# Optimization experiments

Measured on AMD Instinct MI355X. Metric: run time of the kernel, lower is better.

## Reference

```python
import jax, jax.numpy as jnp
import numpy as np

# --- static forest structure: NT complete ternary trees of depth DEPTH ---
BR, DEPTH, NT = 3, 7, 64            # branching factor (=L), edge-levels, num trees
OFF = [(3 ** d - 1) // 2 for d in range(DEPTH + 2)]  # BFS level offsets within a tree
NPT = OFF[DEPTH + 1]                 # nodes per tree = 3280
DIM = NT * NPT                       # total nodes = 209920
C_DIM, NGEN, M_SYM = 8, 8, 128


def build_tree():
    """Returns pos, leaves, batch, roots, levels [(parent_idx, child_idx)], unique-parents per level."""
    base = (np.arange(NT) * NPT)[:, None]
    pos = np.zeros(DIM, dtype=np.int64)
    levels, upar = [], []
    for d in range(1, DEPTH + 1):
        loc = np.arange(OFF[d], OFF[d + 1])
        ch = (base + loc).ravel()                                 # children at depth d (tree-major)
        pa = (base + (OFF[d - 1] + (loc - OFF[d]) // BR)).ravel() # their parents
        pos[ch] = np.tile((loc - OFF[d]) % BR, NT)
        levels.append((pa, ch))
        upar.append((base + np.arange(OFF[d - 1], OFF[d])).ravel())  # unique parents of level d
    leaves = (base + np.arange(OFF[DEPTH], OFF[DEPTH + 1])).ravel()
    batch = np.repeat(np.arange(NT), NPT)
    roots = np.arange(NT) * NPT
    return pos, leaves, batch, roots, levels, upar


def setup_inputs() -> dict:
    key = jax.random.key(0)
    k1, k2, k3, k4, k5 = jax.random.split(key, 5)
    pos_np, leaves_np, batch_np, _, _, _ = build_tree()
    return {
        "lam_A": jax.random.uniform(k1, (C_DIM, C_DIM, BR, NGEN), dtype=jnp.float32),
        "lam_B": jax.random.uniform(k2, (C_DIM, M_SYM, NGEN), dtype=jnp.float32),
        "lam_Pi": jax.random.uniform(k3, (C_DIM, BR, NGEN), dtype=jnp.float32),
        "lam_SP": jax.random.uniform(k4, (BR, NGEN), dtype=jnp.float32),
        "x": jax.random.randint(k5, (DIM,), 0, M_SYM, dtype=jnp.int64),
        "pos": jnp.asarray(pos_np),
        "leaves": jnp.asarray(leaves_np),
        "batch": jnp.asarray(batch_np),
    }


def reference(lam_A, lam_B, lam_Pi, lam_SP, x, pos, leaves, batch):
    # ReversedUpwardDownward (mode='bu') of PosteriorHiddenTreeMarkovModel.
    A = jax.nn.softmax(lam_A, axis=0)   # (C,C,L,G): softmax over first state axis
    Bm = jax.nn.softmax(lam_B, axis=1)  # (C,M,G): softmax over symbols
    Pi = jax.nn.softmax(lam_Pi, axis=0) # (C,L,G)
    SP = jax.nn.softmax(lam_SP, axis=0) # (L,G)
    C, G = A.shape[0], A.shape[-1]
    _, _, _, roots, levels, upar = build_tree()  # static structure

    beta = jnp.zeros((DIM, C, G), lam_A.dtype)
    t_beta = jnp.zeros((DIM, C, G), lam_A.dtype)

    # --- leaves init ---
    Pi_leaves = Pi[:, pos[leaves]]            # (C,Nl,G)
    bl = jnp.transpose(Pi_leaves * Bm[:, x[leaves]], (1, 0, 2))  # (Nl,C,G)
    beta = beta.at[leaves].set(bl / bl.sum(1, keepdims=True))

    # --- upward pass (deepest level first) ---
    for (pa, ch), u in zip(reversed(levels), reversed(upar)):
        SP_ch = SP[pos[ch]][:, None, None, :]                 # (E,1,1,G)
        A_ch = jnp.transpose(A[:, :, pos[ch]], (2, 0, 1, 3))  # (E,C,C,G)
        tb = (SP_ch * A_ch * beta[ch][:, None]).sum(2)        # (E,C,G) sum over child state
        t_beta = t_beta.at[pa].add(tb)
        bu = t_beta[u] * jnp.transpose(Bm[:, x[u]], (1, 0, 2))
        beta = beta.at[u].set(bu / bu.sum(1, keepdims=True))

    # --- downward pass ---
    eps = jnp.zeros((DIM, C, G), lam_A.dtype)
    ell = jnp.zeros((DIM, G), lam_A.dtype)
    eps = eps.at[roots].set(beta[roots])
    for pa, ch in levels:
        SP_ch = SP[pos[ch]]                                   # (E,G)
        A_ch = jnp.transpose(A[:, :, pos[ch]], (2, 0, 1, 3))  # (E,C,C,G)
        trans = SP_ch[:, None, None, :] * A_ch
        ej = (eps[pa][:, :, None, :] * trans * beta[ch][:, None, :, :]
              / t_beta[pa][:, :, None, :])                    # (E,C,C,G) joint posterior
        eps = eps.at[ch].set(ej.sum(1))
        ell = ell.at[ch].add((ej * jnp.log(A_ch)).sum((1, 2))
                             + ej.sum((1, 2)) * jnp.log(SP_ch))
    ell = ell + (eps * jnp.transpose(Bm[:, x], (1, 0, 2))).sum(1)
    ell = ell.at[leaves].add((eps[leaves] * jnp.transpose(jnp.log(Pi_leaves), (1, 0, 2))).sum(1))
    return -jax.ops.segment_sum(ell, batch, num_segments=NT)  # (NT,G)
```

## Files before the change

### kernel.cpp

```cpp
#include <hip/hip_runtime.h>


namespace {

constexpr int kNPT = 3280;
constexpr int kRS  = 72;
constexpr unsigned kMAGIC  = 0x13579BDFu;
constexpr unsigned kMAGIC2 = 0x2468ACEFu;
__device__ __constant__ int LO[6] = {0, 1, 4, 13, 40, 121};
__device__ __constant__ int P3[5] = {1, 3, 9, 27, 81};

#define AGENT_LD(p)    __hip_atomic_load((p), __ATOMIC_RELAXED, __HIP_MEMORY_SCOPE_AGENT)
#define AGENT_ST(p, v) __hip_atomic_store((p), (v), __ATOMIC_RELAXED, __HIP_MEMORY_SCOPE_AGENT)

__device__ __forceinline__ void leaf_beta(const float* __restrict__ sPi,
                                          const float* __restrict__ pBm,
                                          int p, int xv, int g, float* b)
{
    float s = 0.f;
    #pragma unroll
    for (int c = 0; c < 8; ++c) {
        b[c] = sPi[(c * 3 + p) * 8 + g] * pBm[xv * 64 + c * 8 + g];
        s += b[c];
    }
    float ig = __builtin_amdgcn_rcpf(s);
    #pragma unroll
    for (int c = 0; c < 8; ++c) b[c] *= ig;
}

__global__ __launch_bounds__(256, 2)
void fused(const float* __restrict__ lamA, const float* __restrict__ lamB,
           const float* __restrict__ lamPi, const float* __restrict__ lamSP,
           const int* __restrict__ x, float* __restrict__ out,
           unsigned* __restrict__ sy, float* __restrict__ bmG,
           float* __restrict__ b3, float* __restrict__ e3)
{
    const int tid = threadIdx.x, w = tid >> 6, lane = tid & 63;
    const int n = lane >> 3, g = lane & 7;
    __shared__ float sA[1536], sALA[1536], sPi[192], sLPi[192], sSP[24], sLSP[24];
    __shared__ float bW[4][40 * kRS];
    __shared__ float bMid[13 * kRS];
    __shared__ unsigned char xW[4][124];
    unsigned* trCnt = sy + 32;
    unsigned* trFlg = sy + 2080;

    if (tid == 0) {
        if (blockIdx.x == 0) {
            for (int i = 0; i < 64; ++i) AGENT_ST(&trCnt[i * 32], 0u);
            __builtin_amdgcn_s_waitcnt(0);
            AGENT_ST(&sy[0], kMAGIC);
        }
        unsigned long sp = 0;
        while (AGENT_LD(&sy[0]) != kMAGIC) {
            if (++sp > (1UL << 24)) break;
            __builtin_amdgcn_s_sleep(2);
        }
    }
    __syncthreads();

    if (blockIdx.x == 0) {
        float* rr = &bW[0][0];
        int row = tid >> 2, part = tid & 3;
        int c = row >> 3, gg = row & 7, m0 = part * 32;
        float mx = -1e30f;
        for (int mm = 0; mm < 32; ++mm)
            mx = fmaxf(mx, lamB[(c * 128 + m0 + mm) * 8 + gg]);
        rr[tid] = mx;
        __syncthreads();
        float m4 = fmaxf(fmaxf(rr[row * 4], rr[row * 4 + 1]),
                         fmaxf(rr[row * 4 + 2], rr[row * 4 + 3]));
        float s = 0.f;
        for (int mm = 0; mm < 32; ++mm)
            s += expf(lamB[(c * 128 + m0 + mm) * 8 + gg] - m4);
        rr[256 + tid] = s;
        __syncthreads();
        float stot = rr[256 + row * 4] + rr[256 + row * 4 + 1]
                   + rr[256 + row * 4 + 2] + rr[256 + row * 4 + 3];
        float inv = 1.f / stot;
        for (int mm = 0; mm < 32; ++mm)
            AGENT_ST(&bmG[(m0 + mm) * 64 + c * 8 + gg],
                     expf(lamB[(c * 128 + m0 + mm) * 8 + gg] - m4) * inv);
        __syncthreads();
        if (tid == 0) AGENT_ST(&sy[4], kMAGIC2);
    }
    for (int col = tid; col < 192; col += 256) {
        int j = col / 24; int rem = col - j * 24; int p = rem >> 3; int gg = rem & 7;
        float v[8]; float mx = -1e30f;
        #pragma unroll
        for (int i = 0; i < 8; ++i) {
            v[i] = lamA[((i * 8 + j) * 3 + p) * 8 + gg];
            mx = fmaxf(mx, v[i]);
        }
        float s = 0.f;
        #pragma unroll
        for (int i = 0; i < 8; ++i) { v[i] = expf(v[i] - mx); s += v[i]; }
        float inv = 1.f / s;
        #pragma unroll
        for (int i = 0; i < 8; ++i) {
            int idx = ((i * 8 + j) * 3 + p) * 8 + gg;
            float sm = v[i] * inv;
            sA[idx]   = sm;
            sALA[idx] = sm * logf(sm);
        }
    }
    for (int col = tid; col < 24; col += 256) {
        int p = col >> 3; int gg = col & 7;
        float v[8]; float mx = -1e30f;
        #pragma unroll
        for (int c = 0; c < 8; ++c) {
            v[c] = lamPi[(c * 3 + p) * 8 + gg];
            mx = fmaxf(mx, v[c]);
        }
        float s = 0.f;
        #pragma unroll
        for (int c = 0; c < 8; ++c) { v[c] = expf(v[c] - mx); s += v[c]; }
        float inv = 1.f / s;
        #pragma unroll
        for (int c = 0; c < 8; ++c) {
            int idx = (c * 3 + p) * 8 + gg;
            float sm = v[c] * inv;
            sPi[idx]  = sm;
            sLPi[idx] = logf(sm);
        }
    }
    if (tid < 8) {
        int gg = tid;
        float v0 = lamSP[gg], v1 = lamSP[8 + gg], v2 = lamSP[16 + gg];
        float mx = fmaxf(v0, fmaxf(v1, v2));
        float e0 = expf(v0 - mx), e1 = expf(v1 - mx), e2 = expf(v2 - mx);
        float inv = 1.f / (e0 + e1 + e2);
        sSP[gg] = e0 * inv; sSP[8 + gg] = e1 * inv; sSP[16 + gg] = e2 * inv;
        sLSP[gg] = logf(e0 * inv); sLSP[8 + gg] = logf(e1 * inv); sLSP[16 + gg] = logf(e2 * inv);
    }
    if (tid == 0) {
        unsigned long sp = 0;
        while (AGENT_LD(&sy[4]) != kMAGIC2) {
            if (++sp > (1UL << 24)) break;
            __builtin_amdgcn_s_sleep(2);
        }
        __threadfence();
    }
    __syncthreads();

    const float* pBm = bmG;
    const int id = blockIdx.x * 4 + w, t = id / 27, q = id % 27, xb = t * kNPT;
    float* bw = &bW[w][0];
    unsigned char* xw = &xW[w][0];

    for (int u = lane; u < 121; u += 64) {
        int gx;
        if (u == 0)       gx = 13 + q;
        else if (u < 4)   gx = 40  + q * 3  + (u - 1);
        else if (u < 13)  gx = 121 + q * 9  + (u - 4);
        else if (u < 40)  gx = 364 + q * 27 + (u - 13);
        else              gx = 1093 + q * 81 + (u - 40);
        xw[u] = (unsigned char)x[xb + gx];
    }
    __builtin_amdgcn_wave_barrier();

    for (int e = 3; e >= 0; --e) {
        int cnt = P3[e];
        for (int base = 0; base < cnt; base += 8) {
            int pi = base + n;
            if (pi < cnt) {
                float acc[8];
                #pragma unroll
                for (int i = 0; i < 8; ++i) acc[i] = 0.f;
                #pragma unroll
                for (int k = 0; k < 3; ++k) {
                    float bj[8];
                    if (e == 3) {
                        leaf_beta(sPi, pBm, k, xw[40 + 3 * pi + k], g, bj);
                    } else {
                        int co = (LO[e + 1] + 3 * pi + k) * kRS + g;
                        #pragma unroll
                        for (int j = 0; j < 8; ++j) bj[j] = bw[co + j * 8];
                    }
                    float spg = sSP[k * 8 + g];
                    #pragma unroll
                    for (int i = 0; i < 8; ++i) {
                        float s = 0.f;
                        #pragma unroll
                        for (int j = 0; j < 8; ++j)
                            s = fmaf(sA[((i * 8 + j) * 3 + k) * 8 + g], bj[j], s);
                        acc[i] = fmaf(spg, s, acc[i]);
                    }
                }
                if (e == 0) {
                    #pragma unroll
                    for (int i = 0; i < 8; ++i) bw[i * 8 + g] = acc[i];
                    int xv = xw[0];
                    float s = 0.f;
                    #pragma unroll
                    for (int i = 0; i < 8; ++i) { acc[i] *= pBm[xv * 64 + i * 8 + g]; s += acc[i]; }
                    float ig = __builtin_amdgcn_rcpf(s);
                    #pragma unroll
                    for (int i = 0; i < 8; ++i)
                        AGENT_ST(&b3[id * 64 + i * 8 + g], acc[i] * ig);
                } else {
                    int slot = LO[e] + pi;
                    int xv = xw[slot];
                    float s = 0.f;
                    #pragma unroll
                    for (int i = 0; i < 8; ++i) { acc[i] *= pBm[xv * 64 + i * 8 + g]; s += acc[i]; }
                    float ig = __builtin_amdgcn_rcpf(s);
                    int bo = slot * kRS + g;
                    #pragma unroll
                    for (int i = 0; i < 8; ++i) bw[bo + i * 8] = acc[i] * ig;
                    bw[slot * kRS + 64 + g] = s;
                }
            }
        }
        __builtin_amdgcn_wave_barrier();
    }
    __builtin_amdgcn_s_waitcnt(0);
    if (lane == 0)
        __hip_atomic_fetch_add(&trCnt[t * 32], 1u, __ATOMIC_RELAXED,
                               __HIP_MEMORY_SCOPE_AGENT);

    if (q == 0) {
        unsigned long sp = 0;
        while (AGENT_LD(&trCnt[t * 32]) < 27u) {
            if (++sp > (1UL << 22)) break;
            __builtin_amdgcn_s_sleep(1);
        }
        float ellm = 0.f;
        for (int f = 2; f >= 0; --f) {
            int cnt = (f == 2) ? 9 : (f == 1 ? 3 : 1);
            int pl0 = (f == 2) ? 4 : (f == 1 ? 1 : 0);
            int cl0 = (f == 1) ? 4 : 1;
            for (int base = 0; base < cnt; base += 8) {
                int pi = base + n;
                if (pi < cnt) {
                    float acc[8];
                    #pragma unroll
                    for (int i = 0; i < 8; ++i) acc[i] = 0.f;
                    #pragma unroll
                    for (int k = 0; k < 3; ++k) {
                        float bj[8];
                        if (f == 2) {
                            float* src = b3 + (t * 27 + 3 * pi + k) * 64 + g;
                            #pragma unroll
                            for (int j = 0; j < 8; ++j) bj[j] = AGENT_LD(&src[j * 8]);
                        } else {
                            int co = (cl0 + 3 * pi + k) * kRS + g;
                            #pragma unroll
                            for (int j = 0; j < 8; ++j) bj[j] = bMid[co + j * 8];
                        }
                        float spg = sSP[k * 8 + g];
                        #pragma unroll
                        for (int i = 0; i < 8; ++i) {
                            float s = 0.f;
                            #pragma unroll
                            for (int j = 0; j < 8; ++j)
                                s = fmaf(sA[((i * 8 + j) * 3 + k) * 8 + g], bj[j], s);
                            acc[i] = fmaf(spg, s, acc[i]);
                        }
                    }
                    int slot = pl0 + pi;
                    int xv = x[xb + slot];
                    float s = 0.f;
                    #pragma unroll
                    for (int i = 0; i < 8; ++i) { acc[i] *= pBm[xv * 64 + i * 8 + g]; s += acc[i]; }
                    float ig = __builtin_amdgcn_rcpf(s);
                    int bo = slot * kRS + g;
                    #pragma unroll
                    for (int i = 0; i < 8; ++i) bMid[bo + i * 8] = acc[i] * ig;
                    bMid[slot * kRS + 64 + g] = s;
                }
            }
            __builtin_amdgcn_wave_barrier();
        }
        if (n == 0) {
            int xv = x[xb];
            float invs = __builtin_amdgcn_rcpf(bMid[64 + g]);
            #pragma unroll
            for (int c = 0; c < 8; ++c)
                ellm += bMid[c * 8 + g] * pBm[xv * 64 + c * 8 + g];
            #pragma unroll
            for (int c = 0; c < 8; ++c)
                bMid[c * 8 + g] = pBm[xv * 64 + c * 8 + g] * invs;
        }
        __builtin_amdgcn_wave_barrier();
        for (int f = 1; f <= 3; ++f) {
            int cnt = (f == 1) ? 3 : (f == 2 ? 9 : 27);
            int cl0 = (f == 1) ? 1 : (f == 2 ? 4 : 13);
            int pl0 = (f == 1) ? 0 : (f == 2 ? 1 : 4);
            for (int base = 0; base < cnt; base += 8) {
                int ci = base + n;
                if (ci < cnt) {
                    int p = ci % 3;
                    int ps = (pl0 + ci / 3) * kRS + g;
                    float r[8];
                    #pragma unroll
                    for (int i = 0; i < 8; ++i) r[i] = bMid[ps + i * 8];
                    float bj[8]; float sv = 0.f;
                    if (f == 3) {
                        float* src = b3 + (t * 27 + ci) * 64 + g;
                        #pragma unroll
                        for (int j = 0; j < 8; ++j) bj[j] = AGENT_LD(&src[j * 8]);
                    } else {
                        int co = (cl0 + ci) * kRS + g;
                        #pragma unroll
                        for (int j = 0; j < 8; ++j) bj[j] = bMid[co + j * 8];
                        sv = bMid[(cl0 + ci) * kRS + 64 + g];
                    }
                    float spg = sSP[p * 8 + g];
                    float esum = 0.f, lg = 0.f;
                    float ev[8];
                    #pragma unroll
                    for (int j = 0; j < 8; ++j) {
                        float s1 = 0.f, s2 = 0.f;
                        #pragma unroll
                        for (int i = 0; i < 8; ++i) {
                            int ai = ((i * 8 + j) * 3 + p) * 8 + g;
                            s1 = fmaf(r[i], sA[ai],   s1);
                            s2 = fmaf(r[i], sALA[ai], s2);
                        }
                        float bs = spg * bj[j];
                        ev[j] = bs * s1;
                        lg    = fmaf(bs, s2, lg);
                        esum += ev[j];
                    }
                    lg = fmaf(esum, sLSP[p * 8 + g], lg);
                    int xv = x[xb + cl0 + ci];
                    float Bmv[8];
                    #pragma unroll
                    for (int c = 0; c < 8; ++c) {
                        Bmv[c] = pBm[xv * 64 + c * 8 + g];
                        lg = fmaf(ev[c], Bmv[c], lg);
                    }
                    if (f == 3) {
                        #pragma unroll
                        for (int j = 0; j < 8; ++j)
                            AGENT_ST(&e3[(t * 27 + ci) * 64 + j * 8 + g], ev[j]);
                    } else {
                        int co = (cl0 + ci) * kRS + g;
                        #pragma unroll
                        for (int j = 0; j < 8; ++j)
                            bMid[co + j * 8] = ev[j] * Bmv[j]
                                * __builtin_amdgcn_rcpf(bj[j] * sv);
                    }
                    ellm += lg;
                }
            }
            __builtin_amdgcn_wave_barrier();
        }
        ellm += __shfl_xor(ellm, 8);
        ellm += __shfl_xor(ellm, 16);
        ellm += __shfl_xor(ellm, 32);
        if (n == 0) atomicAdd(&out[t * 8 + g], -ellm);
        __builtin_amdgcn_s_waitcnt(0);
        if (lane == 0) AGENT_ST(&trFlg[t * 32], kMAGIC2);
    }

    {
        unsigned long sp = 0;
        while (AGENT_LD(&trFlg[t * 32]) != kMAGIC2) {
            if (++sp > (1UL << 22)) break;
            __builtin_amdgcn_s_sleep(1);
        }
    }
    bw[lane] = AGENT_LD(&e3[id * 64 + lane]) * __builtin_amdgcn_rcpf(bw[lane]);
    __builtin_amdgcn_wave_barrier();

    float ell = 0.f;
    for (int e = 1; e <= 4; ++e) {
        int cnt = P3[e], pl0 = LO[e - 1];
        for (int base = 0; base < cnt; base += 8) {
            int ci = base + n;
            if (ci < cnt) {
                int p = ci % 3;
                int ps = (pl0 + ci / 3) * kRS + g;
                float r[8];
                #pragma unroll
                for (int i = 0; i < 8; ++i) r[i] = bw[ps + i * 8];
                float bj[8]; float sv = 0.f;
                int xv;
                if (e == 4) {
                    xv = xw[40 + ci];
                    leaf_beta(sPi, pBm, p, xv, g, bj);
                } else {
                    int slot = LO[e] + ci;
                    xv = xw[slot];
                    int co = slot * kRS + g;
                    #pragma unroll
                    for (int j = 0; j < 8; ++j) bj[j] = bw[co + j * 8];
                    sv = bw[slot * kRS + 64 + g];
                }
                float spg = sSP[p * 8 + g];
                float esum = 0.f, lg = 0.f;
                float ev[8];
                #pragma unroll
                for (int j = 0; j < 8; ++j) {
                    float s1 = 0.f, s2 = 0.f;
                    #pragma unroll
                    for (int i = 0; i < 8; ++i) {
                        int ai = ((i * 8 + j) * 3 + p) * 8 + g;
                        s1 = fmaf(r[i], sA[ai],   s1);
                        s2 = fmaf(r[i], sALA[ai], s2);
                    }
                    float bs = spg * bj[j];
                    ev[j] = bs * s1;
                    lg    = fmaf(bs, s2, lg);
                    esum += ev[j];
                }
                lg = fmaf(esum, sLSP[p * 8 + g], lg);
                float Bmv[8];
                #pragma unroll
                for (int c = 0; c < 8; ++c) {
                    Bmv[c] = pBm[xv * 64 + c * 8 + g];
                    lg = fmaf(ev[c], Bmv[c], lg);
                }
                if (e < 4) {
                    int slot = LO[e] + ci;
                    int co = slot * kRS + g;
                    #pragma unroll
                    for (int j = 0; j < 8; ++j)
                        bw[co + j * 8] = ev[j] * Bmv[j]
                            * __builtin_amdgcn_rcpf(bj[j] * sv);
                } else {
                    #pragma unroll
                    for (int c = 0; c < 8; ++c)
                        lg = fmaf(ev[c], sLPi[(c * 3 + p) * 8 + g], lg);
                }
                ell += lg;
            }
        }
        __builtin_amdgcn_wave_barrier();
    }

    ell += __shfl_xor(ell, 8);
    ell += __shfl_xor(ell, 16);
    ell += __shfl_xor(ell, 32);
    if (n == 0) atomicAdd(&out[t * 8 + g], -ell);
}

}

extern "C" void kernel_launch(void* const* d_in, const int* in_sizes, int n_in,
                              void* d_out, int out_size, void* d_ws, size_t ws_size,
                              hipStream_t stream) {
    const float* lamA  = (const float*)d_in[0];
    const float* lamB  = (const float*)d_in[1];
    const float* lamPi = (const float*)d_in[2];
    const float* lamSP = (const float*)d_in[3];
    const int*   x     = (const int*)d_in[4];
    float* out = (float*)d_out;
    unsigned* sy  = (unsigned*)d_ws;
    float* bmG = (float*)d_ws + 8192;
    float* b3  = bmG + 8192;
    float* e3  = b3 + 1728 * 64;

    fused<<<dim3(432), dim3(256), 0, stream>>>(
        lamA, lamB, lamPi, lamSP, x, out, sy, bmG, b3, e3);
}
```

Before: 156.6 us.

## Split each subtree across two waves and store mid-tree beta in fp16

Each 81-leaf subtree is now processed by a pair of waves instead of one, with nodes interleaved between the two waves and wave barriers replaced by block-wide syncthreads. The grid doubles to 864 blocks and launch bounds allow 4 blocks per CU. Shared memory shrinks: per-block subtree buffers drop to two, and the top-of-tree mid buffer is stored as half precision with separate float scale sums. The aim is more parallelism and occupancy during the per-subtree passes, at the cost of block-level sync overhead, twice as many blocks spinning on the global flags, and reduced precision in the top-level intermediates.

```diff
diff --git a/kernel.cpp b/kernel.cpp
--- a/kernel.cpp
+++ b/kernel.cpp
@@ -1,4 +1,5 @@
 #include <hip/hip_runtime.h>
+#include <hip/hip_fp16.h>
 
 
 namespace {
@@ -28,7 +29,7 @@
     for (int c = 0; c < 8; ++c) b[c] *= ig;
 }
 
-__global__ __launch_bounds__(256, 2)
+__global__ __launch_bounds__(256, 4)
 void fused(const float* __restrict__ lamA, const float* __restrict__ lamB,
            const float* __restrict__ lamPi, const float* __restrict__ lamSP,
            const int* __restrict__ x, float* __restrict__ out,
@@ -37,10 +38,12 @@
 {
     const int tid = threadIdx.x, w = tid >> 6, lane = tid & 63;
     const int n = lane >> 3, g = lane & 7;
+    const int sub = w >> 1, h = w & 1;
     __shared__ float sA[1536], sALA[1536], sPi[192], sLPi[192], sSP[24], sLSP[24];
-    __shared__ float bW[4][40 * kRS];
-    __shared__ float bMid[13 * kRS];
-    __shared__ unsigned char xW[4][124];
+    __shared__ float bW[2][40 * kRS];
+    __shared__ __half bMidH[13 * 64];
+    __shared__ float sMs[13 * 8];
+    __shared__ unsigned char xW[2][124];
     unsigned* trCnt = sy + 32;
     unsigned* trFlg = sy + 2080;
 
@@ -143,9 +146,9 @@
     __syncthreads();
 
     const float* pBm = bmG;
-    const int id = blockIdx.x * 4 + w, t = id / 27, q = id % 27, xb = t * kNPT;
-    float* bw = &bW[w][0];
-    unsigned char* xw = &xW[w][0];
+    const int id = blockIdx.x * 2 + sub, t = id / 27, q = id % 27, xb = t * kNPT;
+    float* bw = &bW[sub][0];
+    unsigned char* xw = &xW[sub][0];
 
     for (int u = lane; u < 121; u += 64) {
         int gx;
@@ -156,13 +159,13 @@
         else              gx = 1093 + q * 81 + (u - 40);
         xw[u] = (unsigned char)x[xb + gx];
     }
-    __builtin_amdgcn_wave_barrier();
+    __syncthreads();
 
     for (int e = 3; e >= 0; --e) {
         int cnt = P3[e];
-        for (int base = 0; base < cnt; base += 8) {
-            int pi = base + n;
-            if (pi < cnt) {
+        for (int base = 0; base < cnt; base += 16) {
+            int node = base + (n << 1) + h;
+            if (node < cnt) {
                 float acc[8];
                 #pragma unroll
                 for (int i = 0; i < 8; ++i) acc[i] = 0.f;
@@ -170,9 +173,9 @@
                 for (int k = 0; k < 3; ++k) {
                     float bj[8];
                     if (e == 3) {
-                        leaf_beta(sPi, pBm, k, xw[40 + 3 * pi + k], g, bj);
+                        leaf_beta(sPi, pBm, k, xw[40 + 3 * node + k], g, bj);
                     } else {
-                        int co = (LO[e + 1] + 3 * pi + k) * kRS + g;
+                        int co = (LO[e + 1] + 3 * node + k) * kRS + g;
                         #pragma unroll
                         for (int j = 0; j < 8; ++j) bj[j] = bw[co + j * 8];
                     }
@@ -198,7 +201,7 @@
                     for (int i = 0; i < 8; ++i)
                         AGENT_ST(&b3[id * 64 + i * 8 + g], acc[i] * ig);
                 } else {
-                    int slot = LO[e] + pi;
+                    int slot = LO[e] + node;
                     int xv = xw[slot];
                     float s = 0.f;
                     #pragma unroll
@@ -211,14 +214,14 @@
                 }
             }
         }
-        __builtin_amdgcn_wave_barrier();
+        __syncthreads();
     }
     __builtin_amdgcn_s_waitcnt(0);
-    if (lane == 0)
+    if (h == 0 && lane == 0)
         __hip_atomic_fetch_add(&trCnt[t * 32], 1u, __ATOMIC_RELAXED,
                                __HIP_MEMORY_SCOPE_AGENT);
 
-    if (q == 0) {
+    if (q == 0 && h == 0) {
         unsigned long sp = 0;
         while (AGENT_LD(&trCnt[t * 32]) < 27u) {
             if (++sp > (1UL << 22)) break;
@@ -243,9 +246,10 @@
                             #pragma unroll
                             for (int j = 0; j < 8; ++j) bj[j] = AGENT_LD(&src[j * 8]);
                         } else {
-                            int co = (cl0 + 3 * pi + k) * kRS + g;
+                            int co = (cl0 + 3 * pi + k) * 64 + g;
                             #pragma unroll
-                            for (int j = 0; j < 8; ++j) bj[j] = bMid[co + j * 8];
+                            for (int j = 0; j < 8; ++j)
+                                bj[j] = __half2float(bMidH[co + j * 8]);
                         }
                         float spg = sSP[k * 8 + g];
                         #pragma unroll
@@ -263,23 +267,24 @@
                     #pragma unroll
                     for (int i = 0; i < 8; ++i) { acc[i] *= pBm[xv * 64 + i * 8 + g]; s += acc[i]; }
                     float ig = __builtin_amdgcn_rcpf(s);
-                    int bo = slot * kRS + g;
-                    #pragma unroll
-                    for (int i = 0; i < 8; ++i) bMid[bo + i * 8] = acc[i] * ig;
-                    bMid[slot * kRS + 64 + g] = s;
+                    int bo = slot * 64 + g;
+                    #pragma unroll
+                    for (int i = 0; i < 8; ++i)
+                        bMidH[bo + i * 8] = __float2half(acc[i] * ig);
+                    sMs[slot * 8 + g] = s;
                 }
             }
             __builtin_amdgcn_wave_barrier();
         }
         if (n == 0) {
             int xv = x[xb];
-            float invs = __builtin_amdgcn_rcpf(bMid[64 + g]);
+            float invs = __builtin_amdgcn_rcpf(sMs[g]);
             #pragma unroll
             for (int c = 0; c < 8; ++c)
-                ellm += bMid[c * 8 + g] * pBm[xv * 64 + c * 8 + g];
+                ellm += __half2float(bMidH[c * 8 + g]) * pBm[xv * 64 + c * 8 + g];
             #pragma unroll
             for (int c = 0; c < 8; ++c)
-                bMid[c * 8 + g] = pBm[xv * 64 + c * 8 + g] * invs;
+                bMidH[c * 8 + g] = __float2half(pBm[xv * 64 + c * 8 + g] * invs);
         }
         __builtin_amdgcn_wave_barrier();
         for (int f = 1; f <= 3; ++f) {
@@ -290,20 +295,20 @@
                 int ci = base + n;
                 if (ci < cnt) {
                     int p = ci % 3;
-                    int ps = (pl0 + ci / 3) * kRS + g;
+                    int ps = (pl0 + ci / 3) * 64 + g;
                     float r[8];
                     #pragma unroll
-                    for (int i = 0; i < 8; ++i) r[i] = bMid[ps + i * 8];
+                    for (int i = 0; i < 8; ++i) r[i] = __half2float(bMidH[ps + i * 8]);
                     float bj[8]; float sv = 0.f;
                     if (f == 3) {
                         float* src = b3 + (t * 27 + ci) * 64 + g;
                         #pragma unroll
                         for (int j = 0; j < 8; ++j) bj[j] = AGENT_LD(&src[j * 8]);
                     } else {
-                        int co = (cl0 + ci) * kRS + g;
-                        #pragma unroll
-                        for (int j = 0; j < 8; ++j) bj[j] = bMid[co + j * 8];
-                        sv = bMid[(cl0 + ci) * kRS + 64 + g];
+                        int co = (cl0 + ci) * 64 + g;
+                        #pragma unroll
+                        for (int j = 0; j < 8; ++j) bj[j] = __half2float(bMidH[co + j * 8]);
+                        sv = sMs[(cl0 + ci) * 8 + g];
                     }
                     float spg = sSP[p * 8 + g];
                     float esum = 0.f, lg = 0.f;
@@ -335,11 +340,11 @@
                         for (int j = 0; j < 8; ++j)
                             AGENT_ST(&e3[(t * 27 + ci) * 64 + j * 8 + g], ev[j]);
                     } else {
-                        int co = (cl0 + ci) * kRS + g;
+                        int co = (cl0 + ci) * 64 + g;
                         #pragma unroll
                         for (int j = 0; j < 8; ++j)
-                            bMid[co + j * 8] = ev[j] * Bmv[j]
-                                * __builtin_amdgcn_rcpf(bj[j] * sv);
+                            bMidH[co + j * 8] = __float2half(
+                                ev[j] * Bmv[j] * __builtin_amdgcn_rcpf(bj[j] * sv));
                     }
                     ellm += lg;
                 }
@@ -361,14 +366,15 @@
             __builtin_amdgcn_s_sleep(1);
         }
     }
-    bw[lane] = AGENT_LD(&e3[id * 64 + lane]) * __builtin_amdgcn_rcpf(bw[lane]);
-    __builtin_amdgcn_wave_barrier();
+    if (h == 0)
+        bw[lane] = AGENT_LD(&e3[id * 64 + lane]) * __builtin_amdgcn_rcpf(bw[lane]);
+    __syncthreads();
 
     float ell = 0.f;
     for (int e = 1; e <= 4; ++e) {
         int cnt = P3[e], pl0 = LO[e - 1];
-        for (int base = 0; base < cnt; base += 8) {
-            int ci = base + n;
+        for (int base = 0; base < cnt; base += 16) {
+            int ci = base + (n << 1) + h;
             if (ci < cnt) {
                 int p = ci % 3;
                 int ps = (pl0 + ci / 3) * kRS + g;
@@ -427,7 +433,7 @@
                 ell += lg;
             }
         }
-        __builtin_amdgcn_wave_barrier();
+        __syncthreads();
     }
 
     ell += __shfl_xor(ell, 8);
@@ -452,6 +458,6 @@
     float* b3  = bmG + 8192;
     float* e3  = b3 + 1728 * 64;
 
-    fused<<<dim3(432), dim3(256), 0, stream>>>(
+    fused<<<dim3(864), dim3(256), 0, stream>>>(
         lamA, lamB, lamPi, lamSP, x, out, sy, bmG, b3, e3);
 }
```

New measurement: 227.3 us. 45.1% more time.
